# Kernel tuning notes

Hardware: AMD Instinct MI355X
Metric: run time of the kernel (lower is better)

The kernel has to match this reference:

```python
import jax, jax.numpy as jnp
import numpy as np
import math

N = 100000      # num vertices
M = 50000       # num hyperedges
NNZ = 800000    # incidence entries
F_IN = 128
NHID = 128
NCLS = 40
DEPTH = 4
ALPHA = 0.1     # restart_alpha
LAMDA = 0.5


def setup_inputs() -> dict:
    key = jax.random.key(0)
    ks = jax.random.split(key, 8)
    x = jax.random.normal(ks[0], (N, F_IN), jnp.float32)
    vertex = jax.random.randint(ks[1], (NNZ,), 0, N)
    edges = jax.random.randint(ks[2], (NNZ,), 0, M)
    s0 = 1.0 / np.sqrt(F_IN)
    sh = 1.0 / np.sqrt(NHID)
    W0 = jax.random.uniform(ks[3], (F_IN, NHID), jnp.float32, -s0, s0)
    b0 = jax.random.uniform(ks[4], (NHID,), jnp.float32, -s0, s0)
    Ws = jax.random.uniform(ks[5], (DEPTH, NHID, NHID), jnp.float32, -sh, sh)
    Wout = jax.random.uniform(ks[6], (NHID, NCLS), jnp.float32, -sh, sh)
    bout = jax.random.uniform(ks[7], (NCLS,), jnp.float32, -sh, sh)
    return {"x": x, "W0": W0, "b0": b0, "Ws": Ws, "Wout": Wout,
            "bout": bout, "vertex": vertex, "edges": edges}


def reference(x, W0, b0, Ws, Wout, bout, vertex, edges):
    ones = jnp.ones((NNZ, 1), x.dtype)
    cnt_e = jnp.maximum(jax.ops.segment_sum(ones, edges, num_segments=M), 1.0)
    cnt_v = jnp.maximum(jax.ops.segment_sum(ones, vertex, num_segments=N), 1.0)

    x = jax.nn.relu(x @ W0 + b0)
    x0 = x
    for i in range(DEPTH):
        beta = math.log(LAMDA / (i + 1) + 1.0)
        # vertex -> edge mean aggregation
        Xve = x[vertex]                                          # [NNZ, NHID]
        Xe = jax.ops.segment_sum(Xve, edges, num_segments=M) / cnt_e
        # edge -> vertex mean aggregation
        Xev = Xe[edges]                                          # [NNZ, NHID]
        Xv = jax.ops.segment_sum(Xev, vertex, num_segments=N) / cnt_v
        # L2 row-normalize with detached scale (use_norm=True)
        norm = jnp.linalg.norm(Xv, axis=1, keepdims=True)
        scale = jax.lax.stop_gradient(jnp.where(norm > 0, 1.0 / norm, 0.0))
        Xv = Xv * scale
        # alpha/beta residual blend (UniGCNII)
        Xi = (1.0 - ALPHA) * Xv + ALPHA * x0
        x = jax.nn.relu((1.0 - beta) * Xi + beta * (Xi @ Ws[i]))
    return x @ Wout + bout
```

## Files before the change

### kernel.cpp

```cpp
#include <hip/hip_runtime.h>

#define NV 100000
#define NE 50000
#define NNZ_C 800000
#define CAP_E 64
#define CAP_V 48
#define NB_E 391
#define NB_V 782
#define CAPB_E 2560
#define CAPB_V 1408
#define OVF_CAP 810000
#define T_ITEMS 2048
#define N_TILES ((NNZ_C + T_ITEMS - 1) / T_ITEMS)

typedef unsigned int uint32;
typedef unsigned short u16;
typedef u16 u16x8 __attribute__((ext_vector_type(8)));
typedef short short8 __attribute__((ext_vector_type(8)));
typedef float floatx16 __attribute__((ext_vector_type(16)));

__device__ __forceinline__ float bf2f(u16 h) {
  return __uint_as_float(((uint32)h) << 16);
}
__device__ __forceinline__ u16 f2bf(float f) {
  uint32 u = __float_as_uint(f);
  u += 0x7FFF + ((u >> 16) & 1);
  return (u16)(u >> 16);
}


__global__ void zero_misc(int* __restrict__ cur, int n,
                          u16* __restrict__ dummyX, u16* __restrict__ dummyXe) {
  int i = blockIdx.x * blockDim.x + threadIdx.x;
  if (i < n) cur[i] = 0;
  if (i < 128) { dummyX[i] = 0; dummyXe[i] = 0; }
}


__global__ __launch_bounds__(256) void scatter_binned(const int* __restrict__ vertex,
                                                      const int* __restrict__ edges,
                                                      int* __restrict__ curE,
                                                      int* __restrict__ curV,
                                                      int* __restrict__ ovfCnt,
                                                      uint32* __restrict__ pairE,
                                                      uint32* __restrict__ pairV,
                                                      uint2* __restrict__ ovfE,
                                                      uint2* __restrict__ ovfV) {
  __shared__ int histE[NB_E], baseE[NB_E];
  __shared__ int histV[NB_V], baseV[NB_V];
  int t = threadIdx.x;
  for (int tile = blockIdx.x; tile < N_TILES; tile += gridDim.x) {
    for (int b = t; b < NB_E; b += 256) histE[b] = 0;
    for (int b = t; b < NB_V; b += 256) histV[b] = 0;
    __syncthreads();
    int base = tile * T_ITEMS;
    int ev[8], vv[8], rE[8], rV[8];
    #pragma unroll
    for (int i = 0; i < 8; i++) {
      int k = base + t + i * 256;
      if (k < NNZ_C) {
        ev[i] = edges[k];
        vv[i] = vertex[k];
        rE[i] = atomicAdd(&histE[ev[i] >> 7], 1);
        rV[i] = atomicAdd(&histV[vv[i] >> 7], 1);
      }
    }
    __syncthreads();
    for (int b = t; b < NB_E; b += 256) {
      int h = histE[b];
      baseE[b] = h ? atomicAdd(&curE[b], h) : 0;
    }
    for (int b = t; b < NB_V; b += 256) {
      int h = histV[b];
      baseV[b] = h ? atomicAdd(&curV[b], h) : 0;
    }
    __syncthreads();
    #pragma unroll
    for (int i = 0; i < 8; i++) {
      int k = base + t + i * 256;
      if (k < NNZ_C) {
        uint32 e = (uint32)ev[i], v = (uint32)vv[i];
        uint32 pkE = ((e & 127u) << 25) | v;
        uint32 pkV = ((v & 127u) << 25) | e;
        int pE = baseE[e >> 7] + rE[i];
        if (pE < CAPB_E) pairE[(size_t)(e >> 7) * CAPB_E + pE] = pkE;
        else { int op = atomicAdd(&ovfCnt[0], 1); if (op < OVF_CAP) ovfE[op] = make_uint2(e >> 7, pkE); }
        int pV = baseV[v >> 7] + rV[i];
        if (pV < CAPB_V) pairV[(size_t)(v >> 7) * CAPB_V + pV] = pkV;
        else { int op = atomicAdd(&ovfCnt[1], 1); if (op < OVF_CAP) ovfV[op] = make_uint2(v >> 7, pkV); }
      }
    }
    __syncthreads();
  }
}

__global__ __launch_bounds__(256) void expand(const uint32* __restrict__ pairs,
                                              const int* __restrict__ cur, int capb,
                                              const uint2* __restrict__ ovf,
                                              const int* __restrict__ ovfCnt,
                                              int* __restrict__ items, int cap,
                                              int* __restrict__ cnt, int nKeys,
                                              int P, int dummy) {
  __shared__ int lcnt[128];
  int b = blockIdx.x, t = threadIdx.x;
  if (t < 128) lcnt[t] = 0;
  __syncthreads();
  int n = min(cur[b], capb);
  const uint32* p = pairs + (size_t)b * capb;
  for (int i = t; i < n; i += 256) {
    uint32 w = p[i];
    int loc = w >> 25;
    int val = (int)(w & 0x1FFFFFFu);
    int r = atomicAdd(&lcnt[loc], 1);
    if (r < cap) items[(size_t)((b << 7) + loc) * cap + r] = val;
  }
  int novf = min(*ovfCnt, OVF_CAP);
  for (int i = t; i < novf; i += 256) {
    uint2 w = ovf[i];
    if ((int)w.x == b) {
      int loc = w.y >> 25;
      int val = (int)(w.y & 0x1FFFFFFu);
      int r = atomicAdd(&lcnt[loc], 1);
      if (r < cap) items[(size_t)((b << 7) + loc) * cap + r] = val;
    }
  }
  __syncthreads();
  if (t < 128) {
    int key = (b << 7) + t;
    if (key < nKeys) {
      int c = lcnt[t];
      cnt[key] = c;
      int cc = min(c, cap);
      int padded = min((max(cc, 1) + P - 1) & ~(P - 1), cap);
      for (int r = cc; r < padded; r++)
        items[(size_t)key * cap + r] = dummy;
    }
  }
}


__global__ void prep_weights(const float* __restrict__ W0, const float* __restrict__ Ws,
                             u16* __restrict__ WT) {
  int idx = blockIdx.x * blockDim.x + threadIdx.x;
  if (idx >= 5 * 16384) return;
  const float betas[4] = {0.4054651081f, 0.2231435513f, 0.1541506798f, 0.1177830357f};
  int sec = idx >> 14;
  int rc = idx & 16383;
  int n = rc >> 7, k = rc & 127;
  float v;
  if (sec == 0) {
    v = W0[k * 128 + n];
  } else {
    int i = sec - 1;
    float b = betas[i];
    v = b * Ws[i * 16384 + k * 128 + n];
    if (k == n) v += 1.0f - b;
  }
  WT[idx] = f2bf(v);
}


__global__ __launch_bounds__(256, 4) void edge_agg(const u16* __restrict__ Xh,
                                                   const int* __restrict__ cntE,
                                                   const int* __restrict__ itemsE,
                                                   u16* __restrict__ Xeh) {
  int g = threadIdx.x >> 4;
  int lane = threadIdx.x & 15;
  int e = blockIdx.x * 16 + g;
  const int* it = itemsE + (size_t)e * CAP_E;
  int4 i0 = *(const int4*)(it);
  int4 i1 = *(const int4*)(it + 4);
  int4 i2 = *(const int4*)(it + 8);
  int4 i3 = *(const int4*)(it + 12);
  int cnt = cntE[e];
  u16x8 r0 = *(const u16x8*)(Xh + (size_t)i0.x * 128 + lane * 8);
  u16x8 r1 = *(const u16x8*)(Xh + (size_t)i0.y * 128 + lane * 8);
  u16x8 r2 = *(const u16x8*)(Xh + (size_t)i0.z * 128 + lane * 8);
  u16x8 r3 = *(const u16x8*)(Xh + (size_t)i0.w * 128 + lane * 8);
  u16x8 r4 = *(const u16x8*)(Xh + (size_t)i1.x * 128 + lane * 8);
  u16x8 r5 = *(const u16x8*)(Xh + (size_t)i1.y * 128 + lane * 8);
  u16x8 r6 = *(const u16x8*)(Xh + (size_t)i1.z * 128 + lane * 8);
  u16x8 r7 = *(const u16x8*)(Xh + (size_t)i1.w * 128 + lane * 8);
  u16x8 r8 = *(const u16x8*)(Xh + (size_t)i2.x * 128 + lane * 8);
  u16x8 r9 = *(const u16x8*)(Xh + (size_t)i2.y * 128 + lane * 8);
  u16x8 rA = *(const u16x8*)(Xh + (size_t)i2.z * 128 + lane * 8);
  u16x8 rB = *(const u16x8*)(Xh + (size_t)i2.w * 128 + lane * 8);
  u16x8 rC = *(const u16x8*)(Xh + (size_t)i3.x * 128 + lane * 8);
  u16x8 rD = *(const u16x8*)(Xh + (size_t)i3.y * 128 + lane * 8);
  u16x8 rE = *(const u16x8*)(Xh + (size_t)i3.z * 128 + lane * 8);
  u16x8 rF = *(const u16x8*)(Xh + (size_t)i3.w * 128 + lane * 8);
  int n16 = (min(cnt, CAP_E) + 15) & ~15;
  int4 p0, p1, p2, p3;
  if (n16 > 16) {
    p0 = *(const int4*)(it + 16);
    p1 = *(const int4*)(it + 20);
    p2 = *(const int4*)(it + 24);
    p3 = *(const int4*)(it + 28);
  }
  float acc[8];
  #pragma unroll
  for (int q = 0; q < 8; q++) {
    float s0 = (bf2f(r0[q]) + bf2f(r1[q])) + (bf2f(r2[q]) + bf2f(r3[q]));
    float s1 = (bf2f(r4[q]) + bf2f(r5[q])) + (bf2f(r6[q]) + bf2f(r7[q]));
    float s2 = (bf2f(r8[q]) + bf2f(r9[q])) + (bf2f(rA[q]) + bf2f(rB[q]));
    float s3 = (bf2f(rC[q]) + bf2f(rD[q])) + (bf2f(rE[q]) + bf2f(rF[q]));
    acc[q] = (s0 + s1) + (s2 + s3);
  }
  int j = 16;
  while (j < n16) {
    u16x8 s0 = *(const u16x8*)(Xh + (size_t)p0.x * 128 + lane * 8);
    u16x8 s1 = *(const u16x8*)(Xh + (size_t)p0.y * 128 + lane * 8);
    u16x8 s2 = *(const u16x8*)(Xh + (size_t)p0.z * 128 + lane * 8);
    u16x8 s3 = *(const u16x8*)(Xh + (size_t)p0.w * 128 + lane * 8);
    u16x8 s4 = *(const u16x8*)(Xh + (size_t)p1.x * 128 + lane * 8);
    u16x8 s5 = *(const u16x8*)(Xh + (size_t)p1.y * 128 + lane * 8);
    u16x8 s6 = *(const u16x8*)(Xh + (size_t)p1.z * 128 + lane * 8);
    u16x8 s7 = *(const u16x8*)(Xh + (size_t)p1.w * 128 + lane * 8);
    u16x8 s8 = *(const u16x8*)(Xh + (size_t)p2.x * 128 + lane * 8);
    u16x8 s9 = *(const u16x8*)(Xh + (size_t)p2.y * 128 + lane * 8);
    u16x8 sA = *(const u16x8*)(Xh + (size_t)p2.z * 128 + lane * 8);
    u16x8 sB = *(const u16x8*)(Xh + (size_t)p2.w * 128 + lane * 8);
    u16x8 sC = *(const u16x8*)(Xh + (size_t)p3.x * 128 + lane * 8);
    u16x8 sD = *(const u16x8*)(Xh + (size_t)p3.y * 128 + lane * 8);
    u16x8 sE = *(const u16x8*)(Xh + (size_t)p3.z * 128 + lane * 8);
    u16x8 sF = *(const u16x8*)(Xh + (size_t)p3.w * 128 + lane * 8);
    j += 16;
    if (j < n16) {
      p0 = *(const int4*)(it + j);
      p1 = *(const int4*)(it + j + 4);
      p2 = *(const int4*)(it + j + 8);
      p3 = *(const int4*)(it + j + 12);
    }
    #pragma unroll
    for (int q = 0; q < 8; q++) {
      float s0x = (bf2f(s0[q]) + bf2f(s1[q])) + (bf2f(s2[q]) + bf2f(s3[q]));
      float s1x = (bf2f(s4[q]) + bf2f(s5[q])) + (bf2f(s6[q]) + bf2f(s7[q]));
      float s2x = (bf2f(s8[q]) + bf2f(s9[q])) + (bf2f(sA[q]) + bf2f(sB[q]));
      float s3x = (bf2f(sC[q]) + bf2f(sD[q])) + (bf2f(sE[q]) + bf2f(sF[q]));
      acc[q] += (s0x + s1x) + (s2x + s3x);
    }
  }
  float inv = 1.f / fmaxf((float)cnt, 1.f);
  u16x8 o;
  #pragma unroll
  for (int q = 0; q < 8; q++) o[q] = f2bf(acc[q] * inv);
  *(u16x8*)(Xeh + (size_t)e * 128 + lane * 8) = o;
}


__global__ __launch_bounds__(256, 7) void gemm_fused(const u16* __restrict__ Xeh,
                                                     const int* __restrict__ cntV,
                                                     const int* __restrict__ itemsV,
                                                     const u16* __restrict__ x0h,
                                                     const u16* __restrict__ WT,
                                                     u16* __restrict__ Yh, int nrows) {
  __shared__ u16 As[32 * 136];
  int t = threadIdx.x;
  int row0 = blockIdx.x * 32;
  int g = t >> 4, lane = t & 15;

  int vcs[2], cnts[2];
  #pragma unroll
  for (int p = 0; p < 2; p++) {
    int v = row0 + p * 16 + g;
    vcs[p] = min(v, nrows - 1);
    cnts[p] = cntV[vcs[p]];
  }
  int4 a0 = *(const int4*)(itemsV + (size_t)vcs[0] * CAP_V);
  int4 a1 = *(const int4*)(itemsV + (size_t)vcs[0] * CAP_V + 4);

  #pragma unroll
  for (int pass = 0; pass < 2; pass++) {
    int v = row0 + pass * 16 + g;
    int vc = vcs[pass];
    int cnt = cnts[pass];
    const int* it = itemsV + (size_t)vc * CAP_V;
    u16x8 r0 = *(const u16x8*)(Xeh + (size_t)a0.x * 128 + lane * 8);
    u16x8 r1 = *(const u16x8*)(Xeh + (size_t)a0.y * 128 + lane * 8);
    u16x8 r2 = *(const u16x8*)(Xeh + (size_t)a0.z * 128 + lane * 8);
    u16x8 r3 = *(const u16x8*)(Xeh + (size_t)a0.w * 128 + lane * 8);
    u16x8 r4 = *(const u16x8*)(Xeh + (size_t)a1.x * 128 + lane * 8);
    u16x8 r5 = *(const u16x8*)(Xeh + (size_t)a1.y * 128 + lane * 8);
    u16x8 r6 = *(const u16x8*)(Xeh + (size_t)a1.z * 128 + lane * 8);
    u16x8 r7 = *(const u16x8*)(Xeh + (size_t)a1.w * 128 + lane * 8);
    u16x8 x0v = *(const u16x8*)(x0h + (size_t)vc * 128 + lane * 8);
    int n8 = (min(cnt, CAP_V) + 7) & ~7;
    int4 b0, b1;
    if (n8 > 8) {
      b0 = *(const int4*)(it + 8);
      b1 = *(const int4*)(it + 12);
    }
    if (pass < 1) {
      const int* itn = itemsV + (size_t)vcs[pass + 1] * CAP_V;
      a0 = *(const int4*)(itn);
      a1 = *(const int4*)(itn + 4);
    }
    float acc[8];
    #pragma unroll
    for (int q = 0; q < 8; q++)
      acc[q] = ((bf2f(r0[q]) + bf2f(r1[q])) + (bf2f(r2[q]) + bf2f(r3[q]))) +
               ((bf2f(r4[q]) + bf2f(r5[q])) + (bf2f(r6[q]) + bf2f(r7[q])));
    int j = 8;
    while (j < n8) {
      u16x8 s0 = *(const u16x8*)(Xeh + (size_t)b0.x * 128 + lane * 8);
      u16x8 s1 = *(const u16x8*)(Xeh + (size_t)b0.y * 128 + lane * 8);
      u16x8 s2 = *(const u16x8*)(Xeh + (size_t)b0.z * 128 + lane * 8);
      u16x8 s3 = *(const u16x8*)(Xeh + (size_t)b0.w * 128 + lane * 8);
      u16x8 s4 = *(const u16x8*)(Xeh + (size_t)b1.x * 128 + lane * 8);
      u16x8 s5 = *(const u16x8*)(Xeh + (size_t)b1.y * 128 + lane * 8);
      u16x8 s6 = *(const u16x8*)(Xeh + (size_t)b1.z * 128 + lane * 8);
      u16x8 s7 = *(const u16x8*)(Xeh + (size_t)b1.w * 128 + lane * 8);
      j += 8;
      if (j < n8) {
        b0 = *(const int4*)(it + j);
        b1 = *(const int4*)(it + j + 4);
      }
      #pragma unroll
      for (int q = 0; q < 8; q++)
        acc[q] += ((bf2f(s0[q]) + bf2f(s1[q])) + (bf2f(s2[q]) + bf2f(s3[q]))) +
                  ((bf2f(s4[q]) + bf2f(s5[q])) + (bf2f(s6[q]) + bf2f(s7[q])));
    }
    float inv = 1.f / fmaxf((float)cnt, 1.f);
    float sq = 0.f;
    #pragma unroll
    for (int q = 0; q < 8; q++) { acc[q] *= inv; sq += acc[q] * acc[q]; }
    sq += __shfl_xor(sq, 1, 64);
    sq += __shfl_xor(sq, 2, 64);
    sq += __shfl_xor(sq, 4, 64);
    sq += __shfl_xor(sq, 8, 64);
    float scale = (sq > 0.f) ? rsqrtf(sq) : 0.f;
    u16x8 o = {0, 0, 0, 0, 0, 0, 0, 0};
    if (v < nrows) {
      #pragma unroll
      for (int q = 0; q < 8; q++)
        o[q] = f2bf(0.9f * acc[q] * scale + 0.1f * bf2f(x0v[q]));
    }
    *(u16x8*)&As[(pass * 16 + g) * 136 + lane * 8] = o;
  }
  __syncthreads();

  int w = t >> 6, lane64 = t & 63;
  int l31 = lane64 & 31, kh = lane64 >> 5;
  floatx16 acc;
  #pragma unroll
  for (int q = 0; q < 16; q++) acc[q] = 0.f;

  const u16* wtb = WT + (size_t)(w * 32 + l31) * 128;
  #pragma unroll
  for (int ks = 0; ks < 8; ks++) {
    int koff = ks * 16 + kh * 8;
    short8 b0 = *(const short8*)(wtb + koff);
    short8 a0 = *(const short8*)&As[l31 * 136 + koff];
    acc = __builtin_amdgcn_mfma_f32_32x32x16_bf16(a0, b0, acc, 0, 0, 0);
  }
  __syncthreads();

  int col = w * 32 + l31;
  #pragma unroll
  for (int reg = 0; reg < 16; reg++) {
    int row = (reg & 3) + 8 * (reg >> 2) + 4 * kh;
    As[row * 136 + col] = f2bf(fmaxf(acc[reg], 0.f));
  }
  __syncthreads();
  #pragma unroll
  for (int i = 0; i < 2; i++) {
    int idx = t + 256 * i;
    int r = idx >> 4, c8 = idx & 15;
    if (row0 + r < nrows)
      *(u16x8*)(Yh + (size_t)(row0 + r) * 128 + c8 * 8) =
          *(const u16x8*)&As[r * 136 + c8 * 8];
  }
}

__global__ __launch_bounds__(256, 4) void gemm_first(const float* __restrict__ A,
                                                     const u16* __restrict__ WT,
                                                     const float* __restrict__ bias,
                                                     u16* __restrict__ Yh,
                                                     u16* __restrict__ Y2h, int nrows) {
  __shared__ u16 As[128 * 136];
  int t = threadIdx.x;
  int row0 = blockIdx.x * 128;
  #pragma unroll
  for (int i = 0; i < 8; i++) {
    int idx = t + 256 * i;
    int r = idx >> 4, c8 = idx & 15;
    u16x8 v = {0, 0, 0, 0, 0, 0, 0, 0};
    if (row0 + r < nrows) {
      const float* p = A + (size_t)(row0 + r) * 128 + c8 * 8;
      float4 a = *(const float4*)p;
      float4 b = *(const float4*)(p + 4);
      v[0] = f2bf(a.x); v[1] = f2bf(a.y); v[2] = f2bf(a.z); v[3] = f2bf(a.w);
      v[4] = f2bf(b.x); v[5] = f2bf(b.y); v[6] = f2bf(b.z); v[7] = f2bf(b.w);
    }
    *(u16x8*)&As[r * 136 + c8 * 8] = v;
  }
  __syncthreads();

  int w = t >> 6, lane = t & 63;
  int l31 = lane & 31, kh = lane >> 5;
  int wr = w >> 1, wc = w & 1;
  floatx16 acc[2][2];
  #pragma unroll
  for (int rt = 0; rt < 2; rt++)
    #pragma unroll
    for (int ct = 0; ct < 2; ct++)
      #pragma unroll
      for (int q = 0; q < 16; q++) acc[rt][ct][q] = 0.f;

  const u16* wtb0 = WT + (size_t)(wc * 64 + l31) * 128;
  const u16* wtb1 = WT + (size_t)(wc * 64 + 32 + l31) * 128;
  #pragma unroll
  for (int ks = 0; ks < 8; ks++) {
    int koff = ks * 16 + kh * 8;
    short8 b0 = *(const short8*)(wtb0 + koff);
    short8 b1 = *(const short8*)(wtb1 + koff);
    short8 a0 = *(const short8*)&As[(wr * 64 + l31) * 136 + koff];
    short8 a1 = *(const short8*)&As[(wr * 64 + 32 + l31) * 136 + koff];
    acc[0][0] = __builtin_amdgcn_mfma_f32_32x32x16_bf16(a0, b0, acc[0][0], 0, 0, 0);
    acc[0][1] = __builtin_amdgcn_mfma_f32_32x32x16_bf16(a0, b1, acc[0][1], 0, 0, 0);
    acc[1][0] = __builtin_amdgcn_mfma_f32_32x32x16_bf16(a1, b0, acc[1][0], 0, 0, 0);
    acc[1][1] = __builtin_amdgcn_mfma_f32_32x32x16_bf16(a1, b1, acc[1][1], 0, 0, 0);
  }
  __syncthreads();

  #pragma unroll
  for (int rt = 0; rt < 2; rt++)
    #pragma unroll
    for (int ct = 0; ct < 2; ct++) {
      int col = wc * 64 + ct * 32 + l31;
      float bv = bias[col];
      #pragma unroll
      for (int reg = 0; reg < 16; reg++) {
        int row = wr * 64 + rt * 32 + (reg & 3) + 8 * (reg >> 2) + 4 * kh;
        As[row * 136 + col] = f2bf(fmaxf(acc[rt][ct][reg] + bv, 0.f));
      }
    }
  __syncthreads();
  #pragma unroll
  for (int i = 0; i < 8; i++) {
    int idx = t + 256 * i;
    int r = idx >> 4, c8 = idx & 15;
    if (row0 + r < nrows) {
      u16x8 v = *(const u16x8*)&As[r * 136 + c8 * 8];
      *(u16x8*)(Yh + (size_t)(row0 + r) * 128 + c8 * 8) = v;
      *(u16x8*)(Y2h + (size_t)(row0 + r) * 128 + c8 * 8) = v;
    }
  }
}


__global__ __launch_bounds__(256) void gemm_out(const u16* __restrict__ Xh,
                                                const float* __restrict__ W,
                                                const float* __restrict__ bias,
                                                float* __restrict__ Y, int nrows) {
  __shared__ float xs[128][36];
  __shared__ float ws[32][44];
  int t = threadIdx.x;
  int tr = t >> 3;
  int tc = t & 7;
  int row0 = blockIdx.x * 128;
  float acc[4][5];
  #pragma unroll
  for (int i = 0; i < 4; i++)
    #pragma unroll
    for (int j = 0; j < 5; j++) acc[i][j] = 0.f;

  for (int k0 = 0; k0 < 128; k0 += 32) {
    #pragma unroll
    for (int i = 0; i < 2; i++) {
      int idx = t + 256 * i;
      int r = idx >> 2, c8 = idx & 3;
      int gr = row0 + r;
      u16x8 v = {0, 0, 0, 0, 0, 0, 0, 0};
      if (gr < nrows) v = *(const u16x8*)(Xh + (size_t)gr * 128 + k0 + c8 * 8);
      #pragma unroll
      for (int q = 0; q < 8; q++) xs[r][c8 * 8 + q] = bf2f(v[q]);
    }
    #pragma unroll
    for (int i = 0; i < 5; i++) {
      int idx = t + 256 * i;
      int r = idx / 40, c = idx % 40;
      ws[r][c] = W[(k0 + r) * 40 + c];
    }
    __syncthreads();
    #pragma unroll
    for (int kk4 = 0; kk4 < 8; kk4++) {
      float4 xv[4];
      #pragma unroll
      for (int i = 0; i < 4; i++) xv[i] = *(const float4*)&xs[tr + 32 * i][kk4 * 4];
      #pragma unroll
      for (int q = 0; q < 4; q++) {
        int kk = kk4 * 4 + q;
        float wv[5];
        #pragma unroll
        for (int j = 0; j < 5; j++) wv[j] = ws[kk][tc * 5 + j];
        #pragma unroll
        for (int i = 0; i < 4; i++) {
          float xq = ((const float*)&xv[i])[q];
          #pragma unroll
          for (int j = 0; j < 5; j++) acc[i][j] += xq * wv[j];
        }
      }
    }
    __syncthreads();
  }
  #pragma unroll
  for (int i = 0; i < 4; i++) {
    int gr = row0 + tr + 32 * i;
    if (gr >= nrows) continue;
    #pragma unroll
    for (int j = 0; j < 5; j++) {
      int c = tc * 5 + j;
      Y[(long)gr * 40 + c] = acc[i][j] + bias[c];
    }
  }
}


extern "C" void kernel_launch(void* const* d_in, const int* in_sizes, int n_in,
                              void* d_out, int out_size, void* d_ws, size_t ws_size,
                              hipStream_t stream) {
  const float* x    = (const float*)d_in[0];
  const float* W0   = (const float*)d_in[1];
  const float* b0   = (const float*)d_in[2];
  const float* Ws   = (const float*)d_in[3];
  const float* Wout = (const float*)d_in[4];
  const float* bout = (const float*)d_in[5];
  const int* vertex = (const int*)d_in[6];
  const int* edges  = (const int*)d_in[7];
  float* out = (float*)d_out;

  char* base = (char*)d_ws;
  size_t o = 0;
  auto alloc = [&](size_t bytes) -> char* {
    char* r = base + o;
    o += (bytes + 255) & ~(size_t)255;
    return r;
  };
  u16* x_curh = (u16*)alloc((size_t)(NV + 1) * 128 * 2);
  u16* x0h    = (u16*)alloc((size_t)NV * 128 * 2);
  u16* Xeh    = (u16*)alloc((size_t)(NE + 1) * 128 * 2);
  u16* WT     = (u16*)alloc((size_t)5 * 16384 * 2);
  int* cntE   = (int*)alloc((size_t)NE * 4);
  int* cntV   = (int*)alloc((size_t)NV * 4);
  int* itemsE = (int*)alloc((size_t)NE * CAP_E * 4);
  int* itemsV = (int*)alloc((size_t)NV * CAP_V * 4);
  uint32* pairE = (uint32*)alloc((size_t)NB_E * CAPB_E * 4);
  uint32* pairV = (uint32*)alloc((size_t)NB_V * CAPB_V * 4);
  uint2* ovfE  = (uint2*)alloc((size_t)OVF_CAP * 8);
  uint2* ovfV  = (uint2*)alloc((size_t)OVF_CAP * 8);
  int* curAll = (int*)alloc((size_t)(NB_E + NB_V + 2) * 4);
  int* curE = curAll;
  int* curV = curAll + NB_E;
  int* ovfCnt = curAll + NB_E + NB_V;

  int nzero = NB_E + NB_V + 2;
  zero_misc<<<(nzero + 255) / 256, 256, 0, stream>>>(curAll, nzero,
                                                     x_curh + (size_t)NV * 128,
                                                     Xeh + (size_t)NE * 128);
  scatter_binned<<<N_TILES, 256, 0, stream>>>(vertex, edges, curE, curV, ovfCnt,
                                              pairE, pairV, ovfE, ovfV);
  expand<<<NB_E, 256, 0, stream>>>(pairE, curE, CAPB_E, ovfE, ovfCnt,
                                   itemsE, CAP_E, cntE, NE, 16, NV);
  expand<<<NB_V, 256, 0, stream>>>(pairV, curV, CAPB_V, ovfV, ovfCnt + 1,
                                   itemsV, CAP_V, cntV, NV, 8, NE);
  prep_weights<<<(5 * 16384 + 255) / 256, 256, 0, stream>>>(W0, Ws, WT);

  int gblocks = (NV + 127) / 128;
  int fblocks = (NV + 31) / 32;
  gemm_first<<<gblocks, 256, 0, stream>>>(x, WT, b0, x_curh, x0h, NV);

  for (int i = 0; i < 4; i++) {
    edge_agg<<<NE / 16, 256, 0, stream>>>(x_curh, cntE, itemsE, Xeh);
    gemm_fused<<<fblocks, 256, 0, stream>>>(Xeh, cntV, itemsV, x0h,
                                            WT + (size_t)(1 + i) * 16384, x_curh, NV);
  }
  gemm_out<<<gblocks, 256, 0, stream>>>(x_curh, Wout, bout, out, NV);
}
```

Measured before the change: 525.3 us.

## Remap vertex gather to 32 lanes per row with 8-byte loads

Reorganizes the gather-and-normalize phase of gemm_fused so each row is handled by 32 lanes loading 4 bf16 values each, with four passes of 8 rows instead of two passes of 16. The explicit software prefetch of the next incidence indices and of the first eight edge rows is dropped for a simple loop, and occupancy hints go from 7 to 6 blocks. The aim is to spread the reduction across more lanes. The cost is twice as many narrower loads, no prefetch, and no clamp or guard for rows beyond nrows, which only holds when the row count divides by 32.

```diff
diff --git a/kernel.cpp b/kernel.cpp
--- a/kernel.cpp
+++ b/kernel.cpp
@@ -16,6 +16,7 @@
 typedef unsigned int uint32;
 typedef unsigned short u16;
 typedef u16 u16x8 __attribute__((ext_vector_type(8)));
+typedef u16 u16x4 __attribute__((ext_vector_type(4)));
 typedef short short8 __attribute__((ext_vector_type(8)));
 typedef float floatx16 __attribute__((ext_vector_type(16)));
 
@@ -248,7 +249,7 @@
 }
 
 
-__global__ __launch_bounds__(256, 7) void gemm_fused(const u16* __restrict__ Xeh,
+__global__ __launch_bounds__(256, 6) void gemm_fused(const u16* __restrict__ Xeh,
                                                      const int* __restrict__ cntV,
                                                      const int* __restrict__ itemsV,
                                                      const u16* __restrict__ x0h,
@@ -257,85 +258,50 @@
   __shared__ u16 As[32 * 136];
   int t = threadIdx.x;
   int row0 = blockIdx.x * 32;
-  int g = t >> 4, lane = t & 15;
-
-  int vcs[2], cnts[2];
-  #pragma unroll
-  for (int p = 0; p < 2; p++) {
-    int v = row0 + p * 16 + g;
-    vcs[p] = min(v, nrows - 1);
-    cnts[p] = cntV[vcs[p]];
-  }
-  int4 a0 = *(const int4*)(itemsV + (size_t)vcs[0] * CAP_V);
-  int4 a1 = *(const int4*)(itemsV + (size_t)vcs[0] * CAP_V + 4);
-
-  #pragma unroll
-  for (int pass = 0; pass < 2; pass++) {
-    int v = row0 + pass * 16 + g;
-    int vc = vcs[pass];
-    int cnt = cnts[pass];
-    const int* it = itemsV + (size_t)vc * CAP_V;
-    u16x8 r0 = *(const u16x8*)(Xeh + (size_t)a0.x * 128 + lane * 8);
-    u16x8 r1 = *(const u16x8*)(Xeh + (size_t)a0.y * 128 + lane * 8);
-    u16x8 r2 = *(const u16x8*)(Xeh + (size_t)a0.z * 128 + lane * 8);
-    u16x8 r3 = *(const u16x8*)(Xeh + (size_t)a0.w * 128 + lane * 8);
-    u16x8 r4 = *(const u16x8*)(Xeh + (size_t)a1.x * 128 + lane * 8);
-    u16x8 r5 = *(const u16x8*)(Xeh + (size_t)a1.y * 128 + lane * 8);
-    u16x8 r6 = *(const u16x8*)(Xeh + (size_t)a1.z * 128 + lane * 8);
-    u16x8 r7 = *(const u16x8*)(Xeh + (size_t)a1.w * 128 + lane * 8);
-    u16x8 x0v = *(const u16x8*)(x0h + (size_t)vc * 128 + lane * 8);
+  int wid = t >> 6;
+  int half = (t >> 5) & 1;
+  int lane = t & 31;
+
+  #pragma unroll
+  for (int pass = 0; pass < 4; pass++) {
+    int r = pass * 8 + wid * 2 + half;
+    int v = row0 + r;
+    int cnt = cntV[v];
+    const int* it = itemsV + (size_t)v * CAP_V;
+    float acc[4] = {0.f, 0.f, 0.f, 0.f};
     int n8 = (min(cnt, CAP_V) + 7) & ~7;
-    int4 b0, b1;
-    if (n8 > 8) {
-      b0 = *(const int4*)(it + 8);
-      b1 = *(const int4*)(it + 12);
-    }
-    if (pass < 1) {
-      const int* itn = itemsV + (size_t)vcs[pass + 1] * CAP_V;
-      a0 = *(const int4*)(itn);
-      a1 = *(const int4*)(itn + 4);
-    }
-    float acc[8];
-    #pragma unroll
-    for (int q = 0; q < 8; q++)
-      acc[q] = ((bf2f(r0[q]) + bf2f(r1[q])) + (bf2f(r2[q]) + bf2f(r3[q]))) +
-               ((bf2f(r4[q]) + bf2f(r5[q])) + (bf2f(r6[q]) + bf2f(r7[q])));
-    int j = 8;
-    while (j < n8) {
-      u16x8 s0 = *(const u16x8*)(Xeh + (size_t)b0.x * 128 + lane * 8);
-      u16x8 s1 = *(const u16x8*)(Xeh + (size_t)b0.y * 128 + lane * 8);
-      u16x8 s2 = *(const u16x8*)(Xeh + (size_t)b0.z * 128 + lane * 8);
-      u16x8 s3 = *(const u16x8*)(Xeh + (size_t)b0.w * 128 + lane * 8);
-      u16x8 s4 = *(const u16x8*)(Xeh + (size_t)b1.x * 128 + lane * 8);
-      u16x8 s5 = *(const u16x8*)(Xeh + (size_t)b1.y * 128 + lane * 8);
-      u16x8 s6 = *(const u16x8*)(Xeh + (size_t)b1.z * 128 + lane * 8);
-      u16x8 s7 = *(const u16x8*)(Xeh + (size_t)b1.w * 128 + lane * 8);
-      j += 8;
-      if (j < n8) {
-        b0 = *(const int4*)(it + j);
-        b1 = *(const int4*)(it + j + 4);
-      }
+    for (int j = 0; j < n8; j += 8) {
+      int4 e0 = *(const int4*)(it + j);
+      int4 e1 = *(const int4*)(it + j + 4);
+      u16x4 r0 = *(const u16x4*)(Xeh + (size_t)e0.x * 128 + lane * 4);
+      u16x4 r1 = *(const u16x4*)(Xeh + (size_t)e0.y * 128 + lane * 4);
+      u16x4 r2 = *(const u16x4*)(Xeh + (size_t)e0.z * 128 + lane * 4);
+      u16x4 r3 = *(const u16x4*)(Xeh + (size_t)e0.w * 128 + lane * 4);
+      u16x4 r4 = *(const u16x4*)(Xeh + (size_t)e1.x * 128 + lane * 4);
+      u16x4 r5 = *(const u16x4*)(Xeh + (size_t)e1.y * 128 + lane * 4);
+      u16x4 r6 = *(const u16x4*)(Xeh + (size_t)e1.z * 128 + lane * 4);
+      u16x4 r7 = *(const u16x4*)(Xeh + (size_t)e1.w * 128 + lane * 4);
       #pragma unroll
-      for (int q = 0; q < 8; q++)
-        acc[q] += ((bf2f(s0[q]) + bf2f(s1[q])) + (bf2f(s2[q]) + bf2f(s3[q]))) +
-                  ((bf2f(s4[q]) + bf2f(s5[q])) + (bf2f(s6[q]) + bf2f(s7[q])));
+      for (int q = 0; q < 4; q++)
+        acc[q] += ((bf2f(r0[q]) + bf2f(r1[q])) + (bf2f(r2[q]) + bf2f(r3[q]))) +
+                  ((bf2f(r4[q]) + bf2f(r5[q])) + (bf2f(r6[q]) + bf2f(r7[q])));
     }
     float inv = 1.f / fmaxf((float)cnt, 1.f);
     float sq = 0.f;
     #pragma unroll
-    for (int q = 0; q < 8; q++) { acc[q] *= inv; sq += acc[q] * acc[q]; }
+    for (int q = 0; q < 4; q++) { acc[q] *= inv; sq += acc[q] * acc[q]; }
     sq += __shfl_xor(sq, 1, 64);
     sq += __shfl_xor(sq, 2, 64);
     sq += __shfl_xor(sq, 4, 64);
     sq += __shfl_xor(sq, 8, 64);
+    sq += __shfl_xor(sq, 16, 64);
     float scale = (sq > 0.f) ? rsqrtf(sq) : 0.f;
-    u16x8 o = {0, 0, 0, 0, 0, 0, 0, 0};
-    if (v < nrows) {
-      #pragma unroll
-      for (int q = 0; q < 8; q++)
-        o[q] = f2bf(0.9f * acc[q] * scale + 0.1f * bf2f(x0v[q]));
-    }
-    *(u16x8*)&As[(pass * 16 + g) * 136 + lane * 8] = o;
+    u16x4 x0v = *(const u16x4*)(x0h + (size_t)v * 128 + lane * 4);
+    u16x4 o;
+    #pragma unroll
+    for (int q = 0; q < 4; q++)
+      o[q] = f2bf(0.9f * acc[q] * scale + 0.1f * bf2f(x0v[q]));
+    *(u16x4*)&As[r * 136 + lane * 4] = o;
   }
   __syncthreads();
 
```

Result: faster. 494.3 us (-5.9%).
